# Kernel optimization log

Hardware: AMD Instinct MI355X
Metric: run time of the kernel (lower is better)

The kernel has to match this reference:

```python
import jax, jax.numpy as jnp
import numpy as np
from jax import lax

HEADS = 8
SHIFTS = 4
WS = 8          # window_size
C = 192         # channels
MID = C // 2    # 96
EPS = 1e-5      # BatchNorm eps (inference mode, running stats)


def _shift_mask(out_c, in_c):
    """ShiftConv2d0 mask: each channel group only sees one shifted tap of the 3x3 kernel."""
    m = np.zeros((out_c, in_c, 3, 3), np.float32)
    g = in_c // 5
    m[:, 0 * g:1 * g, 1, 2] = 1.0
    m[:, 1 * g:2 * g, 1, 0] = 1.0
    m[:, 2 * g:3 * g, 2, 1] = 1.0
    m[:, 3 * g:4 * g, 0, 1] = 1.0
    m[:, 4 * g:, 1, 1] = 1.0
    return jnp.asarray(m)


def _shift_conv(x, w, b, mask):
    y = lax.conv_general_dilated(x, w * mask, (1, 1), ((1, 1), (1, 1)),
                                 dimension_numbers=('NCHW', 'OIHW', 'NCHW'))
    return y + b[None, :, None, None]


def _bn(x, gamma, beta, mean, var):
    scale = gamma / jnp.sqrt(var + EPS)
    return (x - mean[None, :, None, None]) * scale[None, :, None, None] + beta[None, :, None, None]


def _to_windows(t):
    # b (head c) (h dh) (w dw) -> (b h w) head (dh dw) c
    b, c, H, W = t.shape
    cph = c // HEADS
    hh, ww = H // WS, W // WS
    t = t.reshape(b, HEADS, cph, hh, WS, ww, WS)
    t = t.transpose(0, 3, 5, 1, 4, 6, 2)  # b hh ww head dh dw c
    return t.reshape(b * hh * ww, HEADS, WS * WS, cph)


def _from_windows(t, b, hh, ww):
    # (b h w) head (dh dw) c -> b (head c) (h dh) (w dw)
    cph = t.shape[-1]
    t = t.reshape(b, hh, ww, HEADS, WS, WS, cph)
    t = t.transpose(0, 3, 6, 1, 4, 2, 5)  # b head c hh dh ww dw
    return t.reshape(b, HEADS * cph, hh * WS, ww * WS)


def setup_inputs() -> dict:
    key = jax.random.key(0)
    ks = jax.random.split(key, 24)
    d = {"x": jax.random.normal(ks[0], (4, C, 256, 256), jnp.float32)}
    i = 1
    for name in ("theta", "phi", "g"):
        d[f"w_{name}"] = jax.random.normal(ks[i], (MID, C, 3, 3), jnp.float32) * 0.05; i += 1
        d[f"b_{name}"] = jax.random.normal(ks[i], (MID,), jnp.float32) * 0.05; i += 1
        d[f"gamma_{name}"] = jax.random.uniform(ks[i], (MID,), jnp.float32) + 0.5; i += 1
        d[f"beta_{name}"] = jax.random.normal(ks[i], (MID,), jnp.float32) * 0.1; i += 1
        d[f"mean_{name}"] = jax.random.normal(ks[i], (MID,), jnp.float32) * 0.1; i += 1
        d[f"var_{name}"] = jax.random.uniform(ks[i], (MID,), jnp.float32) + 0.5; i += 1
    d["w_out"] = jax.random.normal(ks[i], (C, MID, 3, 3), jnp.float32) * 0.05; i += 1
    d["b_out"] = jax.random.normal(ks[i], (C,), jnp.float32) * 0.05
    return d


def reference(x, w_theta, b_theta, gamma_theta, beta_theta, mean_theta, var_theta,
              w_phi, b_phi, gamma_phi, beta_phi, mean_phi, var_phi,
              w_g, b_g, gamma_g, beta_g, mean_g, var_g,
              w_out, b_out):
    mask_in = _shift_mask(MID, C)
    mask_out = _shift_mask(C, MID)
    S = SHIFTS
    xp = jnp.pad(x, ((0, 0), (0, 0), (S, S), (S, S)))
    b, _, H, W = xp.shape
    hh, ww = H // WS, W // WS

    theta = _bn(_shift_conv(xp, w_theta, b_theta, mask_in), gamma_theta, beta_theta, mean_theta, var_theta)
    phi = _bn(_shift_conv(xp, w_phi, b_phi, mask_in), gamma_phi, beta_phi, mean_phi, var_phi)
    g = _bn(_shift_conv(xp, w_g, b_g, mask_in), gamma_g, beta_g, mean_g, var_g)

    q = _to_windows(theta)  # [BW, head, WS*WS, c]
    k = _to_windows(phi)
    v = _to_windows(g)

    sim = jnp.einsum('nhqc,nhkc->nhqk', q, k)  # no 1/sqrt(d) scaling in original
    attn = jax.nn.softmax(sim, axis=-1)
    out = jnp.einsum('nhqk,nhkc->nhqc', attn, v)

    out = _from_windows(out, b, hh, ww)
    out = _shift_conv(out, w_out, b_out, mask_out)
    return out[:, :, S:-S, S:-S]
```

## Files before the change

### kernel.cpp

```cpp
#include <hip/hip_runtime.h>
#include <math.h>

typedef unsigned int  uint32;
typedef unsigned short u16;
typedef __attribute__((ext_vector_type(8))) short short8;
typedef __attribute__((ext_vector_type(4))) float f32x4;
typedef __attribute__((ext_vector_type(16))) float f32x16;
typedef __attribute__((ext_vector_type(4))) unsigned int u32x4;

#define NB     4
#define CIN    192
#define MID_C  96
#define OC3    288
#define HH     33
#define NWIN   (NB*HH*HH)
#define PADW   264
#define IMGW   256

__device__ __forceinline__ u16 f2bf(float f) {
    union { float f; uint32 u; } v; v.f = f;
    uint32 u = v.u;
    return (u16)((u + 0x7fffu + ((u >> 16) & 1u)) >> 16);
}
__device__ __forceinline__ float bf_lo(uint32 u) {
    union { uint32 u; float f; } v; v.u = (u << 16); return v.f;
}
__device__ __forceinline__ float bf_hi(uint32 u) {
    union { uint32 u; float f; } v; v.u = (u & 0xffff0000u); return v.f;
}
__device__ __forceinline__ float hi_trunc_f(uint32 u) {
    union { uint32 u; float f; } v; v.u = (u & 0xffff0000u); return v.f;
}
__device__ __forceinline__ uint32 cvtpk_bf16(float a, float b) {
    uint32 r;
    asm("v_cvt_pk_bf16_f32 %0, %1, %2" : "=v"(r) : "v"(a), "v"(b));
    return r;
}

struct PrepArgs {
    const float* w[3];
    const float* b[3];
    const float* gamma[3];
    const float* beta[3];
    const float* mean[3];
    const float* var[3];
    const float* w_out;
    const float* b_out;
    u16*   Wbf;
    u16*   WbfO;
    float* beff;
    float* bout;
};

__global__ __launch_bounds__(256) void prep_kernel(PrepArgs a) {
    int i = blockIdx.x * 256 + threadIdx.x;
    const int khs[5] = {1,1,2,0,1};
    const int kws[5] = {2,0,1,1,1};
    if (i < 288*192) {
        int oc = i / 192, c = i % 192;
        int t = oc / 96, och = oc % 96;
        int grp = (c < 152) ? (c / 38) : 4;
        float scale = a.gamma[t][och] / sqrtf(a.var[t][och] + 1e-5f);
        float v = a.w[t][(och*192 + c)*9 + khs[grp]*3 + kws[grp]] * scale;
        a.Wbf[i] = f2bf(v);
    } else if (i < 288*192 + 192*96) {
        int j = i - 288*192;
        int o = j / 96, c = j % 96;
        int grp = (c < 76) ? (c / 19) : 4;
        a.WbfO[j] = f2bf(a.w_out[(o*96 + c)*9 + khs[grp]*3 + kws[grp]]);
    } else if (i < 288*192 + 192*96 + 480) {
        int j = i - (288*192 + 192*96);
        if (j < 288) {
            int t = j / 96, och = j % 96;
            float scale = a.gamma[t][och] / sqrtf(a.var[t][och] + 1e-5f);
            a.beff[j] = a.beta[t][och] + (a.b[t][och] - a.mean[t][och]) * scale;
        } else {
            a.bout[j - 288] = a.b_out[j - 288];
        }
    }
}

__global__ __launch_bounds__(256, 3) void qkv_attn_kernel(
    const float* __restrict__ x,
    const u16*   __restrict__ Wbf,
    const float* __restrict__ beff,
    u16*         __restrict__ attn_sp)
{
    __shared__ __align__(16) uint32 xs_t[100*36];
    __shared__ __align__(16) u16 qkv[3][64][98];
    __shared__ int shoff[192];

    int blk = blockIdx.x;
    int b   = blk / (HH*HH);
    int rem = blk % (HH*HH);
    int wy  = rem / HH;
    int wx  = rem % HH;
    int tid = threadIdx.x;
    int lane = tid & 63;
    int nt   = __builtin_amdgcn_readfirstlane(tid >> 6);
    int l15  = lane & 15;
    int quad = lane >> 4;

    if (tid < 192) {
        int c = tid;
        int grp = (c < 152) ? (c / 38) : 4;
        int dy = 0, dx = 0;
        if (grp == 0) dx = 1; else if (grp == 1) dx = -1;
        else if (grp == 2) dy = 1; else if (grp == 3) dy = -1;
        shoff[c] = dy*10 + dx;
    }

    int px    = nt*16 + l15;
    int pbase = (1 + (px >> 3))*10 + 1 + (px & 7);

    int gy0 = wy*8 - 1;
    int gx0 = wx*8 - 1;
    const bool border = (wy == 0) || (wy == 32) || (wx == 0) || (wx == 32);

    const int cs  = tid >> 3;
    const int pb8 = tid & 7;
    int   goff[13];
    float emul[13];
    #pragma unroll
    for (int k = 0; k < 13; ++k) {
        int pos = pb8 + 8*k;
        int pp  = (pos < 100) ? pos : 99;
        int r   = pp / 10, col = pp % 10;
        int gy  = gy0 + r, gx = gx0 + col;
        bool valid = (gy >= 4) && (gy < 260) && (gx >= 4) && (gx < 260);
        int cgy = min(max(gy, 4), 259);
        int cgx = min(max(gx, 4), 259);
        goff[k] = cs*65536 + (cgy - 4)*256 + (cgx - 4);
        emul[k] = valid ? 1.f : 0.f;
    }

    const float* xb = x + (size_t)(b*CIN)*65536;

    f32x4 acc[18];
    #pragma unroll
    for (int mt = 0; mt < 18; ++mt) acc[mt] = (f32x4){0.f, 0.f, 0.f, 0.f};

    float bufA[13], bufB[13];

    auto LOADX = [&](float* buf, int chunk) {
        const float* bp = xb + chunk*(32*65536);
        #pragma unroll
        for (int k = 0; k < 12; ++k) buf[k] = bp[goff[k]];
        if (pb8 < 4) buf[12] = bp[goff[12]];
    };

    auto STOREX = [&](float* buf, int chunk) {
        int sh = shoff[chunk*32 + cs];
        if (border) {
            #pragma unroll
            for (int k = 0; k < 12; ++k) buf[k] *= emul[k];
            if (pb8 < 4) buf[12] *= emul[12];
        }
        #pragma unroll
        for (int kk = 0; kk < 6; ++kk) {
            float v0 = buf[2*kk], v1 = buf[2*kk+1];
            uint32 ph = cvtpk_bf16(v0, v1);
            uint32 pl = cvtpk_bf16(v0 - bf_lo(ph), v1 - bf_hi(ph));
            uint32 w0 = (ph & 0xffffu) | (pl << 16);
            uint32 w1 = (ph >> 16)     | (pl & 0xffff0000u);
            int d0 = pb8 + 16*kk - sh;
            int d1 = pb8 + 16*kk + 8 - sh;
            if ((unsigned)d0 < 100u) xs_t[d0*36 + cs] = w0;
            if ((unsigned)d1 < 100u) xs_t[d1*36 + cs] = w1;
        }
        if (pb8 < 4) {
            float v = buf[12];
            uint32 ph = cvtpk_bf16(v, v);
            uint32 pl = cvtpk_bf16(v - bf_lo(ph), 0.f);
            int d = pb8 + 96 - sh;
            if ((unsigned)d < 100u) xs_t[d*36 + cs] = (ph & 0xffffu) | (pl << 16);
        }
    };

    const u32x4* bp128 = (const u32x4*)&xs_t[pbase*36 + quad*8];

    auto COMPUTE = [&](int chunk) {
        u32x4 w0 = bp128[0], w1 = bp128[1];
        short8 bh, bl;
        #pragma unroll
        for (int j = 0; j < 4; ++j) {
            bh[j]   = (short)(u16)(w0[j] & 0xffffu);
            bl[j]   = (short)(u16)(w0[j] >> 16);
            bh[4+j] = (short)(u16)(w1[j] & 0xffffu);
            bl[4+j] = (short)(u16)(w1[j] >> 16);
        }
        const u16* Abase = Wbf + l15*192 + chunk*32 + quad*8;
        #pragma unroll
        for (int mt = 0; mt < 18; ++mt) {
            short8 af = *(const short8*)(Abase + mt*16*192);
            acc[mt] = __builtin_amdgcn_mfma_f32_16x16x32_bf16(af, bh, acc[mt], 0, 0, 0);
            acc[mt] = __builtin_amdgcn_mfma_f32_16x16x32_bf16(af, bl, acc[mt], 0, 0, 0);
        }
    };

    LOADX(bufA, 0);
    #pragma unroll
    for (int cpair = 0; cpair < 3; ++cpair) {
        const int c0 = cpair*2;
        LOADX(bufB, c0 + 1);
        __syncthreads();
        STOREX(bufA, c0);
        __syncthreads();
        COMPUTE(c0);
        if (cpair < 2) LOADX(bufA, c0 + 2);
        __syncthreads();
        STOREX(bufB, c0 + 1);
        __syncthreads();
        COMPUTE(c0 + 1);
    }

    #pragma unroll
    for (int mt = 0; mt < 18; ++mt) {
        #pragma unroll
        for (int r = 0; r < 4; ++r) {
            int oc  = mt*16 + quad*4 + r;
            int t   = oc / 96;
            int och = oc % 96;
            qkv[t][px][och] = f2bf(acc[mt][r] + beff[oc]);
        }
    }
    __syncthreads();

    {
        const int l31 = lane & 31;
        const int hl  = lane >> 5;
        const int vcl = (l31 < 12) ? l31 : 11;

        #pragma unroll
        for (int hrep = 0; hrep < 2; ++hrep) {
            const int head  = nt*2 + hrep;
            const int cbase = head*12 + hl*8;

            auto ldf = [&](const u16* p) -> short8 {
                const uint32* w = (const uint32*)p;
                union { u32x4 u; short8 s; } t_;
                t_.u[0] = w[0];
                t_.u[1] = w[1];
                t_.u[2] = hl ? 0u : w[2];
                t_.u[3] = hl ? 0u : w[3];
                return t_.s;
            };
            short8 kf0 = ldf(&qkv[1][l31][cbase]);
            short8 kf1 = ldf(&qkv[1][32 + l31][cbase]);
            short8 qf0 = ldf(&qkv[0][l31][cbase]);
            short8 qf1 = ldf(&qkv[0][32 + l31][cbase]);

            f32x16 z;
            #pragma unroll
            for (int i = 0; i < 16; ++i) z[i] = 0.f;

            f32x16 sA0 = __builtin_amdgcn_mfma_f32_32x32x16_bf16(kf0, qf0, z, 0, 0, 0);
            f32x16 sB0 = __builtin_amdgcn_mfma_f32_32x32x16_bf16(kf1, qf0, z, 0, 0, 0);
            f32x16 sA1 = __builtin_amdgcn_mfma_f32_32x32x16_bf16(kf0, qf1, z, 0, 0, 0);
            f32x16 sB1 = __builtin_amdgcn_mfma_f32_32x32x16_bf16(kf1, qf1, z, 0, 0, 0);

            auto softmax_col = [&](f32x16& SA, f32x16& SB) {
                float m0 = fmaxf(SA[0], SB[0]);
                float m1 = fmaxf(SA[1], SB[1]);
                float m2 = fmaxf(SA[2], SB[2]);
                float m3 = fmaxf(SA[3], SB[3]);
                #pragma unroll
                for (int i = 4; i < 16; i += 4) {
                    m0 = fmaxf(m0, fmaxf(SA[i+0], SB[i+0]));
                    m1 = fmaxf(m1, fmaxf(SA[i+1], SB[i+1]));
                    m2 = fmaxf(m2, fmaxf(SA[i+2], SB[i+2]));
                    m3 = fmaxf(m3, fmaxf(SA[i+3], SB[i+3]));
                }
                float mx = fmaxf(fmaxf(m0, m1), fmaxf(m2, m3));
                mx = fmaxf(mx, __shfl_xor(mx, 32));
                float s0 = 0.f, s1 = 0.f, s2 = 0.f, s3 = 0.f;
                #pragma unroll
                for (int i = 0; i < 16; i += 4) {
                    SA[i+0] = __expf(SA[i+0] - mx); s0 += SA[i+0];
                    SA[i+1] = __expf(SA[i+1] - mx); s1 += SA[i+1];
                    SA[i+2] = __expf(SA[i+2] - mx); s2 += SA[i+2];
                    SA[i+3] = __expf(SA[i+3] - mx); s3 += SA[i+3];
                    SB[i+0] = __expf(SB[i+0] - mx); s0 += SB[i+0];
                    SB[i+1] = __expf(SB[i+1] - mx); s1 += SB[i+1];
                    SB[i+2] = __expf(SB[i+2] - mx); s2 += SB[i+2];
                    SB[i+3] = __expf(SB[i+3] - mx); s3 += SB[i+3];
                }
                float sum = (s0 + s1) + (s2 + s3);
                sum += __shfl_xor(sum, 32);
                float inv = 1.f / sum;
                #pragma unroll
                for (int i = 0; i < 16; ++i) { SA[i] *= inv; SB[i] *= inv; }
            };
            softmax_col(sA0, sB0);
            softmax_col(sA1, sB1);

            f32x16 o0 = z, o1 = z;
            #pragma unroll
            for (int ks = 0; ks < 4; ++ks) {
                short8 vf;
                #pragma unroll
                for (int j = 0; j < 8; ++j)
                    vf[j] = (short)qkv[2][ks*16 + hl*8 + j][head*12 + vcl];

                auto pv_step = [&](const f32x16& S, f32x16& O) {
                    const int base = (ks & 1) * 8;
                    float p0 = S[base+0], p1 = S[base+1], p2 = S[base+2], p3 = S[base+3];
                    float p4 = S[base+4], p5 = S[base+5], p6 = S[base+6], p7 = S[base+7];
                    uint32 u0 = __float_as_uint(p0), u1 = __float_as_uint(p1);
                    uint32 u2 = __float_as_uint(p2), u3 = __float_as_uint(p3);
                    uint32 u4 = __float_as_uint(p4), u5 = __float_as_uint(p5);
                    uint32 u6 = __float_as_uint(p6), u7 = __float_as_uint(p7);
                    uint32 h0_01 = (u1 & 0xffff0000u) | (u0 >> 16);
                    uint32 h0_23 = (u3 & 0xffff0000u) | (u2 >> 16);
                    uint32 h1_01 = (u5 & 0xffff0000u) | (u4 >> 16);
                    uint32 h1_23 = (u7 & 0xffff0000u) | (u6 >> 16);
                    uint32 l0_01 = (uint32)f2bf(p0 - hi_trunc_f(u0)) | ((uint32)f2bf(p1 - hi_trunc_f(u1)) << 16);
                    uint32 l0_23 = (uint32)f2bf(p2 - hi_trunc_f(u2)) | ((uint32)f2bf(p3 - hi_trunc_f(u3)) << 16);
                    uint32 l1_01 = (uint32)f2bf(p4 - hi_trunc_f(u4)) | ((uint32)f2bf(p5 - hi_trunc_f(u5)) << 16);
                    uint32 l1_23 = (uint32)f2bf(p6 - hi_trunc_f(u6)) | ((uint32)f2bf(p7 - hi_trunc_f(u7)) << 16);
                    uint32 kh01 = hl ? h1_01 : h0_01, kh23 = hl ? h1_23 : h0_23;
                    uint32 sh01 = hl ? h0_01 : h1_01, sh23 = hl ? h0_23 : h1_23;
                    uint32 kl01 = hl ? l1_01 : l0_01, kl23 = hl ? l1_23 : l0_23;
                    uint32 sl01 = hl ? l0_01 : l1_01, sl23 = hl ? l0_23 : l1_23;
                    uint32 rh01 = __shfl_xor(sh01, 32);
                    uint32 rh23 = __shfl_xor(sh23, 32);
                    uint32 rl01 = __shfl_xor(sl01, 32);
                    uint32 rl23 = __shfl_xor(sl23, 32);
                    union { u32x4 u; short8 s; } fh, fl;
                    fh.u[0] = hl ? rh01 : kh01;  fh.u[1] = hl ? rh23 : kh23;
                    fh.u[2] = hl ? kh01 : rh01;  fh.u[3] = hl ? kh23 : rh23;
                    fl.u[0] = hl ? rl01 : kl01;  fl.u[1] = hl ? rl23 : kl23;
                    fl.u[2] = hl ? kl01 : rl01;  fl.u[3] = hl ? kl23 : rl23;
                    O = __builtin_amdgcn_mfma_f32_32x32x16_bf16(fh.s, vf, O, 0, 0, 0);
                    O = __builtin_amdgcn_mfma_f32_32x32x16_bf16(fl.s, vf, O, 0, 0, 0);
                };
                if (ks < 2) { pv_step(sA0, o0); pv_step(sA1, o1); }
                else        { pv_step(sB0, o0); pv_step(sB1, o1); }
            }

            if (l31 < 12) {
                u16* ob = attn_sp + (((b*MID_C + head*12 + l31)*PADW + wy*8)*PADW + wx*8);
                #pragma unroll
                for (int r = 0; r < 16; r += 2) {
                    const int c0  = (r & 3) + 8*(r >> 2);
                    const int pyw = c0 >> 3;
                    const int pxw = (c0 & 7) + 4*hl;
                    *(uint32*)&ob[pyw*PADW + pxw]     = cvtpk_bf16(o0[r], o0[r+1]);
                    *(uint32*)&ob[(pyw+4)*PADW + pxw] = cvtpk_bf16(o1[r], o1[r+1]);
                }
            }
        }
    }
}

__global__ __launch_bounds__(256, 3) void outconv_kernel(
    const u16*   __restrict__ sp,
    const u16*   __restrict__ WbfO,
    const float* __restrict__ bout,
    float*       __restrict__ out)
{
    __shared__ __align__(16) u16 xs_t[200][104];

    int blk = blockIdx.x;
    int b   = blk >> 9;
    int rem = blk & 511;
    int ty  = rem >> 4;
    int tx  = rem & 15;
    int tid = threadIdx.x;
    int lane = tid & 63;
    int ntw  = __builtin_amdgcn_readfirstlane(tid >> 6);
    int l15  = lane & 15;
    int quad = lane >> 4;

    int py0  = ty*8 + 3;
    int px0m = tx*16 + 2;

    int c0 = (tid >> 5) * 12;
    int shm[12];
    #pragma unroll
    for (int m = 0; m < 12; ++m) {
        int c = c0 + m;
        int grp = (c < 76) ? (c / 19) : 4;
        int dy = 0, dx = 0;
        if (grp == 0) dx = 1; else if (grp == 1) dx = -1;
        else if (grp == 2) dy = 1; else if (grp == 3) dy = -1;
        shm[m] = dy*20 + dx;
    }

    {
        const uint32* spu = (const uint32*)sp;
        int u = tid & 31;
        #pragma unroll
        for (int j = 0; j < 4; ++j) {
            int uu = u + 32*j;
            if (uu < 100) {
                int r = uu / 10, w10 = uu % 10;
                int rb = (((py0 + r)*PADW + px0m) >> 1) + w10;
                int pos0 = r*20 + 2*w10;
                #pragma unroll
                for (int m = 0; m < 12; ++m) {
                    int c = c0 + m;
                    uint32 wv = spu[(b*MID_C + c)*34848 + rb];
                    int d0 = pos0 - shm[m];
                    int d1 = pos0 + 1 - shm[m];
                    if ((unsigned)d0 < 200u) xs_t[d0][c] = (u16)(wv & 0xffffu);
                    if ((unsigned)d1 < 200u) xs_t[d1][c] = (u16)(wv >> 16);
                }
            }
        }
    }
    __syncthreads();

    f32x4 acc[3][8];
    #pragma unroll
    for (int mt = 0; mt < 3; ++mt)
        #pragma unroll
        for (int np = 0; np < 8; ++np) acc[mt][np] = (f32x4){0.f, 0.f, 0.f, 0.f};

    #pragma unroll
    for (int ks = 0; ks < 3; ++ks) {
        short8 bfr[8];
        #pragma unroll
        for (int np = 0; np < 8; ++np) {
            int pb = (1 + np)*20 + 2 + l15;
            bfr[np] = *(const short8*)&xs_t[pb][ks*32 + quad*8];
        }
        const u16* Ab = WbfO + (ntw*48)*96 + l15*96 + ks*32 + quad*8;
        #pragma unroll
        for (int mt = 0; mt < 3; ++mt) {
            short8 af = *(const short8*)(Ab + mt*16*96);
            #pragma unroll
            for (int np = 0; np < 8; ++np)
                acc[mt][np] = __builtin_amdgcn_mfma_f32_16x16x32_bf16(af, bfr[np], acc[mt][np], 0, 0, 0);
        }
    }

    int oxb = tx*16 + l15;
    #pragma unroll
    for (int mt = 0; mt < 3; ++mt) {
        #pragma unroll
        for (int rr = 0; rr < 4; ++rr) {
            int oc = ntw*48 + mt*16 + quad*4 + rr;
            float bo = bout[oc];
            #pragma unroll
            for (int np = 0; np < 8; ++np) {
                int oy = ty*8 + np;
                out[((b*CIN + oc)*IMGW + oy)*IMGW + oxb] = acc[mt][np][rr] + bo;
            }
        }
    }
}

extern "C" void kernel_launch(void* const* d_in, const int* in_sizes, int n_in,
                              void* d_out, int out_size, void* d_ws, size_t ws_size,
                              hipStream_t stream) {
    const float* x = (const float*)d_in[0];

    PrepArgs a;
    for (int t = 0; t < 3; ++t) {
        a.w[t]     = (const float*)d_in[1 + 6*t];
        a.b[t]     = (const float*)d_in[2 + 6*t];
        a.gamma[t] = (const float*)d_in[3 + 6*t];
        a.beta[t]  = (const float*)d_in[4 + 6*t];
        a.mean[t]  = (const float*)d_in[5 + 6*t];
        a.var[t]   = (const float*)d_in[6 + 6*t];
    }
    a.w_out = (const float*)d_in[19];
    a.b_out = (const float*)d_in[20];

    char* ws = (char*)d_ws;
    u16*   Wbf     = (u16*)ws;
    u16*   WbfO    = (u16*)(ws + 110592);
    float* beff    = (float*)(ws + 147456);
    float* bout    = (float*)(ws + 148608);
    u16*   attn_sp = (u16*)(ws + 149504);

    a.Wbf = Wbf; a.WbfO = WbfO; a.beff = beff; a.bout = bout;

    const int prep_items = 288*192 + 192*96 + 480;
    prep_kernel<<<(prep_items + 255)/256, 256, 0, stream>>>(a);
    qkv_attn_kernel<<<NWIN, 256, 0, stream>>>(x, Wbf, beff, attn_sp);
    outconv_kernel<<<NB*32*16, 256, 0, stream>>>(attn_sp, WbfO, bout, (float*)d_out);
}
```

Baseline: 754.4 us.

## Alias QKV LDS onto input tile, transpose V, shrink outconv tile

In the QKV/attention kernel the input staging buffer and the q/k buffers now share one LDS region, with an extra barrier before the epilogue writes. V is stored transposed so each PV fragment is one vector load instead of eight scalar LDS reads. The global load mapping changes from channel-per-thread-group to a linear index over channel×position, which should coalesce reads better. The out-conv kernel drops unused halo rows from its LDS tile and reorders its loops so A fragments are held and B fragments streamed, cutting LDS use and register pressure at the cost of more per-element shift lookups.

```diff
diff --git a/kernel.cpp b/kernel.cpp
--- a/kernel.cpp
+++ b/kernel.cpp
@@ -86,9 +86,11 @@
     const float* __restrict__ beff,
     u16*         __restrict__ attn_sp)
 {
-    __shared__ __align__(16) uint32 xs_t[100*36];
-    __shared__ __align__(16) u16 qkv[3][64][98];
+    __shared__ __align__(16) char smem[38912];
     __shared__ int shoff[192];
+    uint32* xs_t = (uint32*)smem;
+    u16 (*qk)[64][98] = (u16 (*)[64][98])smem;
+    u16 (*v_t)[72]    = (u16 (*)[72])(smem + 25088);
 
     int blk = blockIdx.x;
     int b   = blk / (HH*HH);
@@ -117,21 +119,23 @@
     int gx0 = wx*8 - 1;
     const bool border = (wy == 0) || (wy == 32) || (wx == 0) || (wx == 32);
 
-    const int cs  = tid >> 3;
-    const int pb8 = tid & 7;
-    int   goff[13];
-    float emul[13];
+    int    goff[13];
+    int    aux[13];
+    uint32 vmask = 0;
     #pragma unroll
     for (int k = 0; k < 13; ++k) {
-        int pos = pb8 + 8*k;
-        int pp  = (pos < 100) ? pos : 99;
-        int r   = pp / 10, col = pp % 10;
+        int p  = tid + (k << 8);
+        int pp = (p < 3200) ? p : 3199;
+        int cc  = pp / 100;
+        int pos = pp % 100;
+        int r   = pos / 10, col = pos % 10;
         int gy  = gy0 + r, gx = gx0 + col;
         bool valid = (gy >= 4) && (gy < 260) && (gx >= 4) && (gx < 260);
         int cgy = min(max(gy, 4), 259);
         int cgx = min(max(gx, 4), 259);
-        goff[k] = cs*65536 + (cgy - 4)*256 + (cgx - 4);
-        emul[k] = valid ? 1.f : 0.f;
+        goff[k] = cc*65536 + (cgy - 4)*256 + (cgx - 4);
+        aux[k]  = (cc << 8) | pos;
+        if (valid) vmask |= (1u << k);
     }
 
     const float* xb = x + (size_t)(b*CIN)*65536;
@@ -146,15 +150,14 @@
         const float* bp = xb + chunk*(32*65536);
         #pragma unroll
         for (int k = 0; k < 12; ++k) buf[k] = bp[goff[k]];
-        if (pb8 < 4) buf[12] = bp[goff[12]];
+        if (tid < 128) buf[12] = bp[goff[12]];
     };
 
     auto STOREX = [&](float* buf, int chunk) {
-        int sh = shoff[chunk*32 + cs];
         if (border) {
             #pragma unroll
-            for (int k = 0; k < 12; ++k) buf[k] *= emul[k];
-            if (pb8 < 4) buf[12] *= emul[12];
+            for (int k = 0; k < 13; ++k)
+                if (!(vmask & (1u << k))) buf[k] = 0.f;
         }
         #pragma unroll
         for (int kk = 0; kk < 6; ++kk) {
@@ -163,17 +166,20 @@
             uint32 pl = cvtpk_bf16(v0 - bf_lo(ph), v1 - bf_hi(ph));
             uint32 w0 = (ph & 0xffffu) | (pl << 16);
             uint32 w1 = (ph >> 16)     | (pl & 0xffff0000u);
-            int d0 = pb8 + 16*kk - sh;
-            int d1 = pb8 + 16*kk + 8 - sh;
-            if ((unsigned)d0 < 100u) xs_t[d0*36 + cs] = w0;
-            if ((unsigned)d1 < 100u) xs_t[d1*36 + cs] = w1;
-        }
-        if (pb8 < 4) {
+            int a0 = aux[2*kk],   ca = a0 >> 8, pa = a0 & 255;
+            int a1 = aux[2*kk+1], cb = a1 >> 8, pb = a1 & 255;
+            int d0 = pa - shoff[chunk*32 + ca];
+            int d1 = pb - shoff[chunk*32 + cb];
+            if ((unsigned)d0 < 100u) xs_t[d0*36 + ca] = w0;
+            if ((unsigned)d1 < 100u) xs_t[d1*36 + cb] = w1;
+        }
+        if (tid < 128) {
             float v = buf[12];
             uint32 ph = cvtpk_bf16(v, v);
             uint32 pl = cvtpk_bf16(v - bf_lo(ph), 0.f);
-            int d = pb8 + 96 - sh;
-            if ((unsigned)d < 100u) xs_t[d*36 + cs] = (ph & 0xffffu) | (pl << 16);
+            int a = aux[12]; int cc = a >> 8, pp = a & 255;
+            int d = pp - shoff[chunk*32 + cc];
+            if ((unsigned)d < 100u) xs_t[d*36 + cc] = (ph & 0xffffu) | (pl << 16);
         }
     };
 
@@ -214,14 +220,20 @@
         COMPUTE(c0 + 1);
     }
 
+    __syncthreads();
     #pragma unroll
     for (int mt = 0; mt < 18; ++mt) {
         #pragma unroll
         for (int r = 0; r < 4; ++r) {
             int oc  = mt*16 + quad*4 + r;
-            int t   = oc / 96;
-            int och = oc % 96;
-            qkv[t][px][och] = f2bf(acc[mt][r] + beff[oc]);
+            u16 h = f2bf(acc[mt][r] + beff[oc]);
+            if (mt < 12) {
+                int t   = mt / 6;
+                int och = oc - t*96;
+                qk[t][px][och] = h;
+            } else {
+                v_t[oc - 192][px] = h;
+            }
         }
     }
     __syncthreads();
@@ -231,7 +243,7 @@
         const int hl  = lane >> 5;
         const int vcl = (l31 < 12) ? l31 : 11;
 
-        #pragma unroll
+        #pragma unroll 1
         for (int hrep = 0; hrep < 2; ++hrep) {
             const int head  = nt*2 + hrep;
             const int cbase = head*12 + hl*8;
@@ -245,10 +257,10 @@
                 t_.u[3] = hl ? 0u : w[3];
                 return t_.s;
             };
-            short8 kf0 = ldf(&qkv[1][l31][cbase]);
-            short8 kf1 = ldf(&qkv[1][32 + l31][cbase]);
-            short8 qf0 = ldf(&qkv[0][l31][cbase]);
-            short8 qf1 = ldf(&qkv[0][32 + l31][cbase]);
+            short8 kf0 = ldf(&qk[1][l31][cbase]);
+            short8 kf1 = ldf(&qk[1][32 + l31][cbase]);
+            short8 qf0 = ldf(&qk[0][l31][cbase]);
+            short8 qf1 = ldf(&qk[0][32 + l31][cbase]);
 
             f32x16 z;
             #pragma unroll
@@ -297,10 +309,7 @@
             f32x16 o0 = z, o1 = z;
             #pragma unroll
             for (int ks = 0; ks < 4; ++ks) {
-                short8 vf;
-                #pragma unroll
-                for (int j = 0; j < 8; ++j)
-                    vf[j] = (short)qkv[2][ks*16 + hl*8 + j][head*12 + vcl];
+                short8 vf = *(const short8*)&v_t[head*12 + vcl][ks*16 + hl*8];
 
                 auto pv_step = [&](const f32x16& S, f32x16& O) {
                     const int base = (ks & 1) * 8;
@@ -359,7 +368,7 @@
     const float* __restrict__ bout,
     float*       __restrict__ out)
 {
-    __shared__ __align__(16) u16 xs_t[200][104];
+    __shared__ __align__(16) u16 xs_t[160][104];
 
     int blk = blockIdx.x;
     int b   = blk >> 9;
@@ -401,10 +410,10 @@
                 for (int m = 0; m < 12; ++m) {
                     int c = c0 + m;
                     uint32 wv = spu[(b*MID_C + c)*34848 + rb];
-                    int d0 = pos0 - shm[m];
-                    int d1 = pos0 + 1 - shm[m];
-                    if ((unsigned)d0 < 200u) xs_t[d0][c] = (u16)(wv & 0xffffu);
-                    if ((unsigned)d1 < 200u) xs_t[d1][c] = (u16)(wv >> 16);
+                    int d0 = pos0 - shm[m] - 20;
+                    int d1 = d0 + 1;
+                    if ((unsigned)d0 < 160u) xs_t[d0][c] = (u16)(wv & 0xffffu);
+                    if ((unsigned)d1 < 160u) xs_t[d1][c] = (u16)(wv >> 16);
                 }
             }
         }
@@ -419,19 +428,17 @@
 
     #pragma unroll
     for (int ks = 0; ks < 3; ++ks) {
-        short8 bfr[8];
+        const u16* Ab = WbfO + (ntw*48)*96 + l15*96 + ks*32 + quad*8;
+        short8 af[3];
+        #pragma unroll
+        for (int mt = 0; mt < 3; ++mt) af[mt] = *(const short8*)(Ab + mt*16*96);
         #pragma unroll
         for (int np = 0; np < 8; ++np) {
-            int pb = (1 + np)*20 + 2 + l15;
-            bfr[np] = *(const short8*)&xs_t[pb][ks*32 + quad*8];
-        }
-        const u16* Ab = WbfO + (ntw*48)*96 + l15*96 + ks*32 + quad*8;
-        #pragma unroll
-        for (int mt = 0; mt < 3; ++mt) {
-            short8 af = *(const short8*)(Ab + mt*16*96);
+            int pb = np*20 + 2 + l15;
+            short8 bf = *(const short8*)&xs_t[pb][ks*32 + quad*8];
             #pragma unroll
-            for (int np = 0; np < 8; ++np)
-                acc[mt][np] = __builtin_amdgcn_mfma_f32_16x16x32_bf16(af, bfr[np], acc[mt][np], 0, 0, 0);
+            for (int mt = 0; mt < 3; ++mt)
+                acc[mt][np] = __builtin_amdgcn_mfma_f32_16x16x32_bf16(af[mt], bf, acc[mt][np], 0, 0, 0);
         }
     }
 
```

Result: slower. 888.4 us (+17.8%).
